# Performance work log

Hardware: AMD Instinct MI355X
Metric: run time of the kernel (lower is better)

## Reference

```python
import jax, jax.numpy as jnp
import numpy as np

N_GROUPS = 32
N_HEADS = 8
GN_EPS = 1e-5


def setup_inputs() -> dict:
    key = jax.random.key(0)
    k1, k2, k3 = jax.random.split(key, 3)
    B, C, H, W = 8, 512, 32, 32
    x = jax.random.normal(k1, (B, C, H, W), dtype=jnp.float32)
    gn_w = jnp.ones((C,), dtype=jnp.float32)
    gn_b = jnp.zeros((C,), dtype=jnp.float32)
    qkv_w = jax.random.normal(k2, (3 * C, C), dtype=jnp.float32) * 0.02
    qkv_b = jnp.zeros((3 * C,), dtype=jnp.float32)
    proj_w = jax.random.normal(k3, (C, C), dtype=jnp.float32) * 0.02
    proj_b = jnp.zeros((C,), dtype=jnp.float32)
    return {"x": x, "gn_w": gn_w, "gn_b": gn_b, "qkv_w": qkv_w,
            "qkv_b": qkv_b, "proj_w": proj_w, "proj_b": proj_b}


def reference(x, gn_w, gn_b, qkv_w, qkv_b, proj_w, proj_b):
    b, c, h, w = x.shape
    t = h * w
    xf = x.reshape(b, c, t)

    # GroupNorm(32, C) over (channel-group, spatial) dims
    xg = xf.reshape(b, N_GROUPS, (c // N_GROUPS) * t)
    mean = jnp.mean(xg, axis=-1, keepdims=True)
    var = jnp.var(xg, axis=-1, keepdims=True)
    normed = ((xg - mean) * jax.lax.rsqrt(var + GN_EPS)).reshape(b, c, t)
    normed = normed * gn_w[None, :, None] + gn_b[None, :, None]

    # 1x1 Conv1d -> matmul over channel dim
    qkv = jnp.einsum('oc,bct->bot', qkv_w, normed) + qkv_b[None, :, None]
    q, k, v = jnp.split(qkv, 3, axis=1)  # each [b, c, t]

    ch = c // N_HEADS
    scale = 1.0 / np.sqrt(np.sqrt(ch)).astype(np.float32)
    q = (q * scale).reshape(b * N_HEADS, ch, t)
    k = (k * scale).reshape(b * N_HEADS, ch, t)
    v = v.reshape(b * N_HEADS, ch, t)

    weight = jnp.einsum('bct,bcs->bts', q, k)
    weight = jax.nn.softmax(weight.astype(jnp.float32), axis=-1).astype(q.dtype)
    a = jnp.einsum('bts,bcs->bct', weight, v).reshape(b, c, t)

    # residual + 1x1 Conv2d projection
    out = jnp.einsum('oc,bct->bot', proj_w, xf + a) + proj_b[None, :, None]
    return out.reshape(b, -1, h, w)
```

## Files before the change

kernel.cpp:

```cpp
#include <hip/hip_runtime.h>

constexpr int B = 8;
constexpr int C = 512;
constexpr int T = 1024;
constexpr int CPG = 16;
constexpr int NH = 8;
constexpr int CH = 64;
constexpr float GN_EPS = 1e-5f;
constexpr float SCALE = 0.35355339059327373f;
constexpr float QSCALE = 0.18033688011112042f;

typedef __attribute__((ext_vector_type(4))) float f32x4;
typedef __attribute__((ext_vector_type(8))) short bf16x8;
typedef __attribute__((ext_vector_type(4))) short bf16x4;

__device__ inline short f2bf(float f) {
  union { float f; unsigned u; } v; v.f = f;
  unsigned r = (v.u + 0x7FFFu + ((v.u >> 16) & 1u)) >> 16;
  return (short)r;
}

__device__ inline unsigned cvt_pk_bf16(float a, float b) {
  unsigned r;
  asm("v_cvt_pk_bf16_f32 %0, %1, %2" : "=v"(r) : "v"(a), "v"(b));
  return r;
}

#define GLOAD16(gsrc, ldst) __builtin_amdgcn_global_load_lds( \
    (const __attribute__((address_space(1))) unsigned int*)(gsrc), \
    (__attribute__((address_space(3))) unsigned int*)(ldst), 16, 0, 0)

__global__ __launch_bounds__(256)
void wconv_kernel(const float* __restrict__ qw, const float* __restrict__ pw,
                  short* __restrict__ qwb, short* __restrict__ pwb) {
  const int idx = blockIdx.x * 256 + threadIdx.x;
  constexpr int QW4 = 3 * C * C / 4;
  float4 v;
  short* dst;
  if (idx < QW4) {
    v = ((const float4*)qw)[idx];
    dst = qwb + (size_t)idx * 4;
  } else {
    v = ((const float4*)pw)[idx - QW4];
    dst = pwb + (size_t)(idx - QW4) * 4;
  }
  bf16x4 o;
  o[0] = f2bf(v.x); o[1] = f2bf(v.y); o[2] = f2bf(v.z); o[3] = f2bf(v.w);
  *(bf16x4*)dst = o;
}

__global__ __launch_bounds__(256)
void gn_kernel(const float* __restrict__ x, const float* __restrict__ gw,
               const float* __restrict__ gb, short* __restrict__ out) {
  const int b = blockIdx.x >> 5;
  const int g = blockIdx.x & 31;
  const float* xp = x + (size_t)(b * C + g * CPG) * T;
  const float4* x4 = (const float4*)xp;
  float s = 0.f, ss = 0.f;
  for (int i = threadIdx.x; i < CPG * T / 4; i += 256) {
    float4 v = x4[i];
    s  += v.x + v.y + v.z + v.w;
    ss += v.x * v.x + v.y * v.y + v.z * v.z + v.w * v.w;
  }
  #pragma unroll
  for (int o = 32; o; o >>= 1) {
    s  += __shfl_down(s, o);
    ss += __shfl_down(ss, o);
  }
  __shared__ float rs[4], rss[4];
  __shared__ float sm, sr;
  const int wid = threadIdx.x >> 6;
  if ((threadIdx.x & 63) == 0) { rs[wid] = s; rss[wid] = ss; }
  __syncthreads();
  if (threadIdx.x == 0) {
    float ts  = rs[0] + rs[1] + rs[2] + rs[3];
    float tss = rss[0] + rss[1] + rss[2] + rss[3];
    constexpr float inv_n = 1.f / (CPG * T);
    float mean = ts * inv_n;
    float var = tss * inv_n - mean * mean;
    sm = mean;
    sr = rsqrtf(var + GN_EPS);
  }
  __syncthreads();
  const float mean = sm, rstd = sr;

  const int tid = threadIdx.x;
  const int cl = tid >> 4;
  const int t4 = (tid & 15) * 4;
  const float cw = gw[g * CPG + cl] * rstd;
  const float cb = gb[g * CPG + cl] - mean * cw;
  __shared__ short tile[64][20];
  const int tr = tid >> 2;
  const int cq = (tid & 3) * 4;
  for (int t0 = 0; t0 < T; t0 += 64) {
    float4 v = x4[(cl * T + t0 + t4) >> 2];
    tile[t4 + 0][cl] = f2bf(v.x * cw + cb);
    tile[t4 + 1][cl] = f2bf(v.y * cw + cb);
    tile[t4 + 2][cl] = f2bf(v.z * cw + cb);
    tile[t4 + 3][cl] = f2bf(v.w * cw + cb);
    __syncthreads();
    *(bf16x4*)&out[((size_t)(b * T + t0 + tr)) * C + g * CPG + cq] =
        *(const bf16x4*)&tile[tr][cq];
    __syncthreads();
  }
}

__global__ __launch_bounds__(256)
void qkv_gemm(const short* __restrict__ Wb, const float* __restrict__ bias,
              const short* __restrict__ Xn, short* __restrict__ qb,
              short* __restrict__ kb, short* __restrict__ vb) {
  const int b = blockIdx.z;
  const int o0 = blockIdx.y * 128;
  const int t0 = blockIdx.x * 128;
  const bool swap = (o0 >= 2 * C);
  __shared__ short Asm[128 * 64];
  __shared__ short Bsm[128 * 64];
  const int tid = threadIdx.x;
  const int wv = tid >> 6, lane = tid & 63;
  const int l15 = lane & 15, l4 = lane >> 4;
  const int wr = (wv >> 1) * 64, wc = (wv & 1) * 64;

  const short* gA[4]; const short* gB[4];
  char* lA[4]; char* lB[4];
  #pragma unroll
  for (int p = 0; p < 4; ++p) {
    const int off = p * 256 + tid;
    const int row = off >> 3;
    const int col = (off & 7) ^ (row & 7);
    gA[p] = Wb + (size_t)(o0 + row) * C + col * 8;
    gB[p] = Xn + ((size_t)b * T + t0 + row) * C + col * 8;
    lA[p] = (char*)Asm + (size_t)(p * 256 + (tid & ~63)) * 16;
    lB[p] = (char*)Bsm + (size_t)(p * 256 + (tid & ~63)) * 16;
  }

  f32x4 acc[4][4];
  #pragma unroll
  for (int i = 0; i < 4; ++i)
    #pragma unroll
    for (int j = 0; j < 4; ++j) acc[i][j] = f32x4{0.f, 0.f, 0.f, 0.f};

  for (int k0 = 0; k0 < C; k0 += 64) {
    #pragma unroll
    for (int p = 0; p < 4; ++p) {
      GLOAD16(gA[p] + k0, lA[p]);
      GLOAD16(gB[p] + k0, lB[p]);
    }
    __syncthreads();
    #pragma unroll
    for (int kk = 0; kk < 2; ++kk) {
      bf16x8 af[4], bfr[4];
      #pragma unroll
      for (int i = 0; i < 4; ++i) {
        const int sw = ((kk << 2) | l4) ^ (l15 & 7);
        af[i]  = *(const bf16x8*)&Asm[(wr + i * 16 + l15) * 64 + sw * 8];
        bfr[i] = *(const bf16x8*)&Bsm[(wc + i * 16 + l15) * 64 + sw * 8];
      }
      if (!swap) {
        #pragma unroll
        for (int fi = 0; fi < 4; ++fi)
          #pragma unroll
          for (int nj = 0; nj < 4; ++nj)
            acc[fi][nj] = __builtin_amdgcn_mfma_f32_16x16x32_bf16(
                af[fi], bfr[nj], acc[fi][nj], 0, 0, 0);
      } else {
        #pragma unroll
        for (int nj = 0; nj < 4; ++nj)
          #pragma unroll
          for (int fi = 0; fi < 4; ++fi)
            acc[nj][fi] = __builtin_amdgcn_mfma_f32_16x16x32_bf16(
                bfr[nj], af[fi], acc[nj][fi], 0, 0, 0);
      }
    }
    __syncthreads();
  }

  if (!swap) {
    short* dst = (o0 < C) ? qb : kb;
    const float sc = (o0 < C) ? QSCALE : 1.0f;
    #pragma unroll
    for (int fi = 0; fi < 4; ++fi) {
      const int ob = o0 + wr + fi * 16 + l4 * 4;
      const int bh = b * NH + ((ob >> 6) & 7);
      const int cb_ = ob & 63;
      #pragma unroll
      for (int nj = 0; nj < 4; ++nj) {
        const int tg = t0 + wc + nj * 16 + l15;
        bf16x4 pk;
        #pragma unroll
        for (int r = 0; r < 4; ++r)
          pk[r] = f2bf((acc[fi][nj][r] + bias[ob + r]) * sc);
        *(bf16x4*)&dst[((size_t)bh * T + tg) * CH + cb_] = pk;
      }
    }
  } else {
    #pragma unroll
    for (int fi = 0; fi < 4; ++fi) {
      const int ob = o0 + wr + fi * 16 + l15;
      const int bh = b * NH + ((ob >> 6) & 7);
      const int cb_ = ob & 63;
      const float bo = bias[ob];
      #pragma unroll
      for (int nj = 0; nj < 4; ++nj) {
        const int tg = t0 + wc + nj * 16 + l4 * 4;
        bf16x4 pk;
        #pragma unroll
        for (int r = 0; r < 4; ++r)
          pk[r] = f2bf(acc[nj][fi][r] + bo);
        *(bf16x4*)&vb[((size_t)bh * CH + cb_) * T + tg] = pk;
      }
    }
  }
}

__global__ __launch_bounds__(256)
void attn_kernel(const short* __restrict__ qb, const short* __restrict__ kb,
                 const short* __restrict__ vb, const float* __restrict__ x,
                 short* __restrict__ res) {
  const int linear = blockIdx.x;
  const int bh = (linear & 7) * 8 + ((linear >> 3) >> 4);
  const int tile = (linear >> 3) & 15;
  const int b = bh >> 3, h = bh & 7;
  const int t0 = tile * 64;
  const int tid = threadIdx.x;
  const int wv = tid >> 6;
  const int lane = tid & 63;
  const int l15 = lane & 15;
  const int l4 = lane >> 4;

  const short* qh = qb + (size_t)bh * T * CH;
  const short* kh = kb + (size_t)bh * T * CH;
  const short* vh = vb + (size_t)bh * CH * T;

  __shared__ short kt[2][64][64];
  __shared__ short vt[2][64][64];
  __shared__ short pl[4][16][64];
  short* plw = &pl[wv][0][0];

  const int sl_row[2] = { (0 * 256 + tid) >> 3, (1 * 256 + tid) >> 3 };
  const int sl_blk[2] = { (tid & 7) ^ (sl_row[0] & 7), (tid & 7) ^ (sl_row[1] & 7) };
  const int sl_lds[2] = { (0 * 256 + (tid & ~63)) * 8, (1 * 256 + (tid & ~63)) * 8 };

  bf16x8 qf[2];
  #pragma unroll
  for (int ks = 0; ks < 2; ++ks)
    qf[ks] = *(const bf16x8*)&qh[(size_t)(t0 + wv * 16 + l15) * CH + ks * 32 + l4 * 8];

  f32x4 acc_o[4];
  #pragma unroll
  for (int ct = 0; ct < 4; ++ct) acc_o[ct] = f32x4{0.f, 0.f, 0.f, 0.f};
  float lsum = 0.f;

  #pragma unroll
  for (int p = 0; p < 2; ++p) {
    GLOAD16(kh + (size_t)sl_row[p] * CH + sl_blk[p] * 8, &kt[0][0][0] + sl_lds[p]);
    GLOAD16(vh + (size_t)sl_row[p] * T + sl_blk[p] * 8, &vt[0][0][0] + sl_lds[p]);
  }

  for (int it = 0; it < 16; ++it) {
    const int cur = it & 1;
    __syncthreads();
    if (it < 15) {
      const int s1 = (it + 1) * 64;
      #pragma unroll
      for (int p = 0; p < 2; ++p) {
        GLOAD16(kh + (size_t)(s1 + sl_row[p]) * CH + sl_blk[p] * 8,
                &kt[cur ^ 1][0][0] + sl_lds[p]);
        GLOAD16(vh + (size_t)sl_row[p] * T + s1 + sl_blk[p] * 8,
                &vt[cur ^ 1][0][0] + sl_lds[p]);
      }
    }
    const short* ktc = &kt[cur][0][0];
    const short* vtc = &vt[cur][0][0];

    f32x4 accs[4];
    #pragma unroll
    for (int nt = 0; nt < 4; ++nt) accs[nt] = f32x4{0.f, 0.f, 0.f, 0.f};
    __builtin_amdgcn_s_setprio(1);
    #pragma unroll
    for (int ks = 0; ks < 2; ++ks) {
      #pragma unroll
      for (int nt = 0; nt < 4; ++nt) {
        bf16x8 kf = *(const bf16x8*)
            &ktc[(nt * 16 + l15) * 64 + (((ks << 2) | l4) ^ (l15 & 7)) * 8];
        accs[nt] = __builtin_amdgcn_mfma_f32_16x16x32_bf16(kf, qf[ks], accs[nt], 0, 0, 0);
      }
    }
    __builtin_amdgcn_s_setprio(0);

    f32x4 p4[4];
    #pragma unroll
    for (int nt = 0; nt < 4; ++nt)
      #pragma unroll
      for (int r = 0; r < 4; ++r)
        p4[nt][r] = __builtin_amdgcn_exp2f(accs[nt][r]);

    {
      f32x4 sv;
      #pragma unroll
      for (int r = 0; r < 4; ++r)
        sv[r] = (p4[0][r] + p4[1][r]) + (p4[2][r] + p4[3][r]);
      lsum += (sv[0] + sv[1]) + (sv[2] + sv[3]);
    }

    #pragma unroll
    for (int nt = 0; nt < 4; ++nt) {
      uint2 w;
      w.x = cvt_pk_bf16(p4[nt][0], p4[nt][1]);
      w.y = cvt_pk_bf16(p4[nt][2], p4[nt][3]);
      *(uint2*)&plw[l15 * 64 + ((nt * 2 + (l4 >> 1)) ^ (l15 & 7)) * 8 + (l4 & 1) * 4] = w;
    }

    __builtin_amdgcn_s_setprio(1);
    #pragma unroll
    for (int ks = 0; ks < 2; ++ks) {
      bf16x8 pf = *(const bf16x8*)
          &plw[l15 * 64 + (((ks << 2) | l4) ^ (l15 & 7)) * 8];
      #pragma unroll
      for (int ct = 0; ct < 4; ++ct) {
        bf16x8 vf = *(const bf16x8*)
            &vtc[(ct * 16 + l15) * 64 + (((ks << 2) | l4) ^ (l15 & 7)) * 8];
        acc_o[ct] = __builtin_amdgcn_mfma_f32_16x16x32_bf16(vf, pf, acc_o[ct], 0, 0, 0);
      }
    }
    __builtin_amdgcn_s_setprio(0);
  }

  float l = lsum;
  l += __shfl_xor(l, 16);
  l += __shfl_xor(l, 32);

  const float inv = 1.f / l;
  const int trow = t0 + wv * 16 + l15;
  #pragma unroll
  for (int ct = 0; ct < 4; ++ct) {
    const int cbase = h * CH + ct * 16 + l4 * 4;
    bf16x4 pk;
    #pragma unroll
    for (int r = 0; r < 4; ++r) {
      const float xv = x[((size_t)(b * C + cbase + r)) * T + trow];
      pk[r] = f2bf(acc_o[ct][r] * inv + xv);
    }
    *(bf16x4*)&res[((size_t)(b * T + trow)) * C + cbase] = pk;
  }
}

__global__ __launch_bounds__(256)
void proj_gemm(const short* __restrict__ Wp, const float* __restrict__ bias,
               const short* __restrict__ Rs, float* __restrict__ out) {
  const int b = blockIdx.z;
  const int o0 = blockIdx.y * 128;
  const int t0 = blockIdx.x * 128;
  __shared__ short Asm[128 * 64];
  __shared__ short Bsm[128 * 64];
  const int tid = threadIdx.x;
  const int wv = tid >> 6, lane = tid & 63;
  const int l15 = lane & 15, l4 = lane >> 4;
  const int wr = (wv >> 1) * 64, wc = (wv & 1) * 64;

  const short* gA[4]; const short* gB[4];
  char* lA[4]; char* lB[4];
  #pragma unroll
  for (int p = 0; p < 4; ++p) {
    const int off = p * 256 + tid;
    const int row = off >> 3;
    const int col = (off & 7) ^ (row & 7);
    gA[p] = Wp + (size_t)(o0 + row) * C + col * 8;
    gB[p] = Rs + ((size_t)b * T + t0 + row) * C + col * 8;
    lA[p] = (char*)Asm + (size_t)(p * 256 + (tid & ~63)) * 16;
    lB[p] = (char*)Bsm + (size_t)(p * 256 + (tid & ~63)) * 16;
  }

  f32x4 acc[4][4];
  #pragma unroll
  for (int i = 0; i < 4; ++i)
    #pragma unroll
    for (int j = 0; j < 4; ++j) acc[i][j] = f32x4{0.f, 0.f, 0.f, 0.f};

  for (int k0 = 0; k0 < C; k0 += 64) {
    #pragma unroll
    for (int p = 0; p < 4; ++p) {
      GLOAD16(gA[p] + k0, lA[p]);
      GLOAD16(gB[p] + k0, lB[p]);
    }
    __syncthreads();
    #pragma unroll
    for (int kk = 0; kk < 2; ++kk) {
      bf16x8 af[4], bfr[4];
      #pragma unroll
      for (int i = 0; i < 4; ++i) {
        const int sw = ((kk << 2) | l4) ^ (l15 & 7);
        af[i]  = *(const bf16x8*)&Asm[(wr + i * 16 + l15) * 64 + sw * 8];
        bfr[i] = *(const bf16x8*)&Bsm[(wc + i * 16 + l15) * 64 + sw * 8];
      }
      #pragma unroll
      for (int nj = 0; nj < 4; ++nj)
        #pragma unroll
        for (int fi = 0; fi < 4; ++fi)
          acc[nj][fi] = __builtin_amdgcn_mfma_f32_16x16x32_bf16(
              bfr[nj], af[fi], acc[nj][fi], 0, 0, 0);
    }
    __syncthreads();
  }

  #pragma unroll
  for (int fi = 0; fi < 4; ++fi) {
    const int o = o0 + wr + fi * 16 + l15;
    const float bo = bias[o];
    #pragma unroll
    for (int nj = 0; nj < 4; ++nj) {
      const int tg = t0 + wc + nj * 16 + l4 * 4;
      f32x4 vo;
      #pragma unroll
      for (int r = 0; r < 4; ++r) vo[r] = acc[nj][fi][r] + bo;
      *(f32x4*)&out[((size_t)(b * C + o)) * T + tg] = vo;
    }
  }
}

extern "C" void kernel_launch(void* const* d_in, const int* in_sizes, int n_in,
                              void* d_out, int out_size, void* d_ws, size_t ws_size,
                              hipStream_t stream) {
  const float* x      = (const float*)d_in[0];
  const float* gn_w   = (const float*)d_in[1];
  const float* gn_b   = (const float*)d_in[2];
  const float* qkv_w  = (const float*)d_in[3];
  const float* qkv_b  = (const float*)d_in[4];
  const float* proj_w = (const float*)d_in[5];
  const float* proj_b = (const float*)d_in[6];
  float* out = (float*)d_out;

  constexpr size_t MB = 1 << 20;
  char* w = (char*)d_ws;
  short* normed = (short*)w;
  short* qbuf   = (short*)(w + 8 * MB);
  short* kbuf   = (short*)(w + 16 * MB);
  short* vbuf   = (short*)(w + 24 * MB);
  short* resb   = (short*)(w + 32 * MB);
  short* qwb    = (short*)(w + 40 * MB);
  short* pwb    = (short*)(w + 40 * MB + (size_t)3 * C * C * 2);

  wconv_kernel<<<dim3(1024), 256, 0, stream>>>(qkv_w, proj_w, qwb, pwb);
  gn_kernel<<<dim3(B * 32), 256, 0, stream>>>(x, gn_w, gn_b, normed);
  qkv_gemm<<<dim3(T / 128, 3 * C / 128, B), 256, 0, stream>>>(qwb, qkv_b, normed,
                                                              qbuf, kbuf, vbuf);
  attn_kernel<<<dim3(B * NH * (T / 64)), 256, 0, stream>>>(qbuf, kbuf, vbuf, x, resb);
  proj_gemm<<<dim3(T / 128, C / 128, B), 256, 0, stream>>>(pwb, proj_b, resb, out);
}
```

Measured before the change: 92.56 us.

## Double-buffer GEMM LDS tiles and double query rows per attention wave

Both the QKV and projection GEMMs now double-buffer their A/B LDS tiles, prefetching the next K slice while MFMAs run on the current one, and raise wave priority around the MFMA blocks. The attention kernel now has each wave handle 32 query rows (two 16-row fragments) instead of 16. Each K/V tile loaded into LDS is therefore reused twice as much, and the grid is halved. The costs are double the LDS per GEMM block, more registers and LDS for the attention kernel, and fewer attention blocks to spread across the CUs.

```diff
diff --git a/kernel.cpp b/kernel.cpp
--- a/kernel.cpp
+++ b/kernel.cpp
@@ -7,7 +7,6 @@
 constexpr int NH = 8;
 constexpr int CH = 64;
 constexpr float GN_EPS = 1e-5f;
-constexpr float SCALE = 0.35355339059327373f;
 constexpr float QSCALE = 0.18033688011112042f;
 
 typedef __attribute__((ext_vector_type(4))) float f32x4;
@@ -113,8 +112,8 @@
   const int o0 = blockIdx.y * 128;
   const int t0 = blockIdx.x * 128;
   const bool swap = (o0 >= 2 * C);
-  __shared__ short Asm[128 * 64];
-  __shared__ short Bsm[128 * 64];
+  __shared__ short Asm[2][128 * 64];
+  __shared__ short Bsm[2][128 * 64];
   const int tid = threadIdx.x;
   const int wv = tid >> 6, lane = tid & 63;
   const int l15 = lane & 15, l4 = lane >> 4;
@@ -129,8 +128,8 @@
     const int col = (off & 7) ^ (row & 7);
     gA[p] = Wb + (size_t)(o0 + row) * C + col * 8;
     gB[p] = Xn + ((size_t)b * T + t0 + row) * C + col * 8;
-    lA[p] = (char*)Asm + (size_t)(p * 256 + (tid & ~63)) * 16;
-    lB[p] = (char*)Bsm + (size_t)(p * 256 + (tid & ~63)) * 16;
+    lA[p] = (char*)&Asm[0][0] + (size_t)(p * 256 + (tid & ~63)) * 16;
+    lB[p] = (char*)&Bsm[0][0] + (size_t)(p * 256 + (tid & ~63)) * 16;
   }
 
   f32x4 acc[4][4];
@@ -139,22 +138,35 @@
     #pragma unroll
     for (int j = 0; j < 4; ++j) acc[i][j] = f32x4{0.f, 0.f, 0.f, 0.f};
 
-  for (int k0 = 0; k0 < C; k0 += 64) {
-    #pragma unroll
-    for (int p = 0; p < 4; ++p) {
-      GLOAD16(gA[p] + k0, lA[p]);
-      GLOAD16(gB[p] + k0, lB[p]);
-    }
-    __syncthreads();
+  #pragma unroll
+  for (int p = 0; p < 4; ++p) {
+    GLOAD16(gA[p], lA[p]);
+    GLOAD16(gB[p], lB[p]);
+  }
+  __syncthreads();
+
+  int cur = 0;
+  for (int ks = 0; ks < 8; ++ks) {
+    if (ks < 7) {
+      const int k0n = (ks + 1) * 64;
+      #pragma unroll
+      for (int p = 0; p < 4; ++p) {
+        GLOAD16(gA[p] + k0n, lA[p] + (cur ^ 1) * 16384);
+        GLOAD16(gB[p] + k0n, lB[p] + (cur ^ 1) * 16384);
+      }
+    }
+    const short* As = &Asm[cur][0];
+    const short* Bs = &Bsm[cur][0];
     #pragma unroll
     for (int kk = 0; kk < 2; ++kk) {
       bf16x8 af[4], bfr[4];
       #pragma unroll
       for (int i = 0; i < 4; ++i) {
         const int sw = ((kk << 2) | l4) ^ (l15 & 7);
-        af[i]  = *(const bf16x8*)&Asm[(wr + i * 16 + l15) * 64 + sw * 8];
-        bfr[i] = *(const bf16x8*)&Bsm[(wc + i * 16 + l15) * 64 + sw * 8];
-      }
+        af[i]  = *(const bf16x8*)&As[(wr + i * 16 + l15) * 64 + sw * 8];
+        bfr[i] = *(const bf16x8*)&Bs[(wc + i * 16 + l15) * 64 + sw * 8];
+      }
+      __builtin_amdgcn_s_setprio(1);
       if (!swap) {
         #pragma unroll
         for (int fi = 0; fi < 4; ++fi)
@@ -170,8 +182,10 @@
             acc[nj][fi] = __builtin_amdgcn_mfma_f32_16x16x32_bf16(
                 bfr[nj], af[fi], acc[nj][fi], 0, 0, 0);
       }
+      __builtin_amdgcn_s_setprio(0);
     }
     __syncthreads();
+    cur ^= 1;
   }
 
   if (!swap) {
@@ -216,11 +230,10 @@
 void attn_kernel(const short* __restrict__ qb, const short* __restrict__ kb,
                  const short* __restrict__ vb, const float* __restrict__ x,
                  short* __restrict__ res) {
-  const int linear = blockIdx.x;
-  const int bh = (linear & 7) * 8 + ((linear >> 3) >> 4);
-  const int tile = (linear >> 3) & 15;
+  const int bh = blockIdx.x & 63;
+  const int tile = blockIdx.x >> 6;
   const int b = bh >> 3, h = bh & 7;
-  const int t0 = tile * 64;
+  const int t0 = tile * 128;
   const int tid = threadIdx.x;
   const int wv = tid >> 6;
   const int lane = tid & 63;
@@ -233,27 +246,32 @@
 
   __shared__ short kt[2][64][64];
   __shared__ short vt[2][64][64];
-  __shared__ short pl[4][16][64];
-  short* plw = &pl[wv][0][0];
+  __shared__ short pl[4][2][16][64];
+  short* plw = &pl[wv][0][0][0];
 
   const int sl_row[2] = { (0 * 256 + tid) >> 3, (1 * 256 + tid) >> 3 };
   const int sl_blk[2] = { (tid & 7) ^ (sl_row[0] & 7), (tid & 7) ^ (sl_row[1] & 7) };
   const int sl_lds[2] = { (0 * 256 + (tid & ~63)) * 8, (1 * 256 + (tid & ~63)) * 8 };
 
-  bf16x8 qf[2];
-  #pragma unroll
-  for (int ks = 0; ks < 2; ++ks)
-    qf[ks] = *(const bf16x8*)&qh[(size_t)(t0 + wv * 16 + l15) * CH + ks * 32 + l4 * 8];
-
-  f32x4 acc_o[4];
-  #pragma unroll
-  for (int ct = 0; ct < 4; ++ct) acc_o[ct] = f32x4{0.f, 0.f, 0.f, 0.f};
-  float lsum = 0.f;
+  bf16x8 qf[2][2];
+  #pragma unroll
+  for (int nj = 0; nj < 2; ++nj)
+    #pragma unroll
+    for (int ks = 0; ks < 2; ++ks)
+      qf[nj][ks] = *(const bf16x8*)
+          &qh[(size_t)(t0 + wv * 32 + nj * 16 + l15) * CH + ks * 32 + l4 * 8];
+
+  f32x4 acc_o[2][4];
+  #pragma unroll
+  for (int nj = 0; nj < 2; ++nj)
+    #pragma unroll
+    for (int ct = 0; ct < 4; ++ct) acc_o[nj][ct] = f32x4{0.f, 0.f, 0.f, 0.f};
+  float lsum[2] = {0.f, 0.f};
 
   #pragma unroll
   for (int p = 0; p < 2; ++p) {
-    GLOAD16(kh + (size_t)sl_row[p] * CH + sl_blk[p] * 8, &kt[0][0][0] + sl_lds[p]);
-    GLOAD16(vh + (size_t)sl_row[p] * T + sl_blk[p] * 8, &vt[0][0][0] + sl_lds[p]);
+    GLOAD16(kh + (size_t)sl_row[p] * CH + sl_blk[p] * 8, (char*)&kt[0][0][0] + sl_lds[p] * 2);
+    GLOAD16(vh + (size_t)sl_row[p] * T + sl_blk[p] * 8, (char*)&vt[0][0][0] + sl_lds[p] * 2);
   }
 
   for (int it = 0; it < 16; ++it) {
@@ -264,17 +282,19 @@
       #pragma unroll
       for (int p = 0; p < 2; ++p) {
         GLOAD16(kh + (size_t)(s1 + sl_row[p]) * CH + sl_blk[p] * 8,
-                &kt[cur ^ 1][0][0] + sl_lds[p]);
+                (char*)&kt[cur ^ 1][0][0] + sl_lds[p] * 2);
         GLOAD16(vh + (size_t)sl_row[p] * T + s1 + sl_blk[p] * 8,
-                &vt[cur ^ 1][0][0] + sl_lds[p]);
+                (char*)&vt[cur ^ 1][0][0] + sl_lds[p] * 2);
       }
     }
     const short* ktc = &kt[cur][0][0];
     const short* vtc = &vt[cur][0][0];
 
-    f32x4 accs[4];
-    #pragma unroll
-    for (int nt = 0; nt < 4; ++nt) accs[nt] = f32x4{0.f, 0.f, 0.f, 0.f};
+    f32x4 accs[2][4];
+    #pragma unroll
+    for (int nj = 0; nj < 2; ++nj)
+      #pragma unroll
+      for (int nt = 0; nt < 4; ++nt) accs[nj][nt] = f32x4{0.f, 0.f, 0.f, 0.f};
     __builtin_amdgcn_s_setprio(1);
     #pragma unroll
     for (int ks = 0; ks < 2; ++ks) {
@@ -282,65 +302,70 @@
       for (int nt = 0; nt < 4; ++nt) {
         bf16x8 kf = *(const bf16x8*)
             &ktc[(nt * 16 + l15) * 64 + (((ks << 2) | l4) ^ (l15 & 7)) * 8];
-        accs[nt] = __builtin_amdgcn_mfma_f32_16x16x32_bf16(kf, qf[ks], accs[nt], 0, 0, 0);
+        accs[0][nt] = __builtin_amdgcn_mfma_f32_16x16x32_bf16(kf, qf[0][ks], accs[0][nt], 0, 0, 0);
+        accs[1][nt] = __builtin_amdgcn_mfma_f32_16x16x32_bf16(kf, qf[1][ks], accs[1][nt], 0, 0, 0);
       }
     }
     __builtin_amdgcn_s_setprio(0);
 
-    f32x4 p4[4];
-    #pragma unroll
-    for (int nt = 0; nt < 4; ++nt)
+    f32x4 p4[2][4];
+    #pragma unroll
+    for (int nj = 0; nj < 2; ++nj) {
+      #pragma unroll
+      for (int nt = 0; nt < 4; ++nt)
+        #pragma unroll
+        for (int r = 0; r < 4; ++r)
+          p4[nj][nt][r] = __builtin_amdgcn_exp2f(accs[nj][nt][r]);
+      f32x4 sv;
       #pragma unroll
       for (int r = 0; r < 4; ++r)
-        p4[nt][r] = __builtin_amdgcn_exp2f(accs[nt][r]);
-
-    {
-      f32x4 sv;
-      #pragma unroll
-      for (int r = 0; r < 4; ++r)
-        sv[r] = (p4[0][r] + p4[1][r]) + (p4[2][r] + p4[3][r]);
-      lsum += (sv[0] + sv[1]) + (sv[2] + sv[3]);
-    }
-
-    #pragma unroll
-    for (int nt = 0; nt < 4; ++nt) {
-      uint2 w;
-      w.x = cvt_pk_bf16(p4[nt][0], p4[nt][1]);
-      w.y = cvt_pk_bf16(p4[nt][2], p4[nt][3]);
-      *(uint2*)&plw[l15 * 64 + ((nt * 2 + (l4 >> 1)) ^ (l15 & 7)) * 8 + (l4 & 1) * 4] = w;
+        sv[r] = (p4[nj][0][r] + p4[nj][1][r]) + (p4[nj][2][r] + p4[nj][3][r]);
+      lsum[nj] += (sv[0] + sv[1]) + (sv[2] + sv[3]);
+      #pragma unroll
+      for (int nt = 0; nt < 4; ++nt) {
+        uint2 w;
+        w.x = cvt_pk_bf16(p4[nj][nt][0], p4[nj][nt][1]);
+        w.y = cvt_pk_bf16(p4[nj][nt][2], p4[nj][nt][3]);
+        *(uint2*)&plw[nj * 1024 + l15 * 64 +
+                      ((nt * 2 + (l4 >> 1)) ^ (l15 & 7)) * 8 + (l4 & 1) * 4] = w;
+      }
     }
 
     __builtin_amdgcn_s_setprio(1);
     #pragma unroll
     for (int ks = 0; ks < 2; ++ks) {
-      bf16x8 pf = *(const bf16x8*)
-          &plw[l15 * 64 + (((ks << 2) | l4) ^ (l15 & 7)) * 8];
+      const int psl = (((ks << 2) | l4) ^ (l15 & 7)) * 8;
+      bf16x8 pf0 = *(const bf16x8*)&plw[l15 * 64 + psl];
+      bf16x8 pf1 = *(const bf16x8*)&plw[1024 + l15 * 64 + psl];
       #pragma unroll
       for (int ct = 0; ct < 4; ++ct) {
         bf16x8 vf = *(const bf16x8*)
             &vtc[(ct * 16 + l15) * 64 + (((ks << 2) | l4) ^ (l15 & 7)) * 8];
-        acc_o[ct] = __builtin_amdgcn_mfma_f32_16x16x32_bf16(vf, pf, acc_o[ct], 0, 0, 0);
+        acc_o[0][ct] = __builtin_amdgcn_mfma_f32_16x16x32_bf16(vf, pf0, acc_o[0][ct], 0, 0, 0);
+        acc_o[1][ct] = __builtin_amdgcn_mfma_f32_16x16x32_bf16(vf, pf1, acc_o[1][ct], 0, 0, 0);
       }
     }
     __builtin_amdgcn_s_setprio(0);
   }
 
-  float l = lsum;
-  l += __shfl_xor(l, 16);
-  l += __shfl_xor(l, 32);
-
-  const float inv = 1.f / l;
-  const int trow = t0 + wv * 16 + l15;
-  #pragma unroll
-  for (int ct = 0; ct < 4; ++ct) {
-    const int cbase = h * CH + ct * 16 + l4 * 4;
-    bf16x4 pk;
-    #pragma unroll
-    for (int r = 0; r < 4; ++r) {
-      const float xv = x[((size_t)(b * C + cbase + r)) * T + trow];
-      pk[r] = f2bf(acc_o[ct][r] * inv + xv);
-    }
-    *(bf16x4*)&res[((size_t)(b * T + trow)) * C + cbase] = pk;
+  #pragma unroll
+  for (int nj = 0; nj < 2; ++nj) {
+    float l = lsum[nj];
+    l += __shfl_xor(l, 16);
+    l += __shfl_xor(l, 32);
+    const float inv = 1.f / l;
+    const int trow = t0 + wv * 32 + nj * 16 + l15;
+    #pragma unroll
+    for (int ct = 0; ct < 4; ++ct) {
+      const int cbase = h * CH + ct * 16 + l4 * 4;
+      bf16x4 pk;
+      #pragma unroll
+      for (int r = 0; r < 4; ++r) {
+        const float xv = x[((size_t)(b * C + cbase + r)) * T + trow];
+        pk[r] = f2bf(acc_o[nj][ct][r] * inv + xv);
+      }
+      *(bf16x4*)&res[((size_t)(b * T + trow)) * C + cbase] = pk;
+    }
   }
 }
 
@@ -350,8 +375,8 @@
   const int b = blockIdx.z;
   const int o0 = blockIdx.y * 128;
   const int t0 = blockIdx.x * 128;
-  __shared__ short Asm[128 * 64];
-  __shared__ short Bsm[128 * 64];
+  __shared__ short Asm[2][128 * 64];
+  __shared__ short Bsm[2][128 * 64];
   const int tid = threadIdx.x;
   const int wv = tid >> 6, lane = tid & 63;
   const int l15 = lane & 15, l4 = lane >> 4;
@@ -366,8 +391,8 @@
     const int col = (off & 7) ^ (row & 7);
     gA[p] = Wp + (size_t)(o0 + row) * C + col * 8;
     gB[p] = Rs + ((size_t)b * T + t0 + row) * C + col * 8;
-    lA[p] = (char*)Asm + (size_t)(p * 256 + (tid & ~63)) * 16;
-    lB[p] = (char*)Bsm + (size_t)(p * 256 + (tid & ~63)) * 16;
+    lA[p] = (char*)&Asm[0][0] + (size_t)(p * 256 + (tid & ~63)) * 16;
+    lB[p] = (char*)&Bsm[0][0] + (size_t)(p * 256 + (tid & ~63)) * 16;
   }
 
   f32x4 acc[4][4];
@@ -376,30 +401,45 @@
     #pragma unroll
     for (int j = 0; j < 4; ++j) acc[i][j] = f32x4{0.f, 0.f, 0.f, 0.f};
 
-  for (int k0 = 0; k0 < C; k0 += 64) {
-    #pragma unroll
-    for (int p = 0; p < 4; ++p) {
-      GLOAD16(gA[p] + k0, lA[p]);
-      GLOAD16(gB[p] + k0, lB[p]);
-    }
-    __syncthreads();
+  #pragma unroll
+  for (int p = 0; p < 4; ++p) {
+    GLOAD16(gA[p], lA[p]);
+    GLOAD16(gB[p], lB[p]);
+  }
+  __syncthreads();
+
+  int cur = 0;
+  for (int ks = 0; ks < 8; ++ks) {
+    if (ks < 7) {
+      const int k0n = (ks + 1) * 64;
+      #pragma unroll
+      for (int p = 0; p < 4; ++p) {
+        GLOAD16(gA[p] + k0n, lA[p] + (cur ^ 1) * 16384);
+        GLOAD16(gB[p] + k0n, lB[p] + (cur ^ 1) * 16384);
+      }
+    }
+    const short* As = &Asm[cur][0];
+    const short* Bs = &Bsm[cur][0];
     #pragma unroll
     for (int kk = 0; kk < 2; ++kk) {
       bf16x8 af[4], bfr[4];
       #pragma unroll
       for (int i = 0; i < 4; ++i) {
         const int sw = ((kk << 2) | l4) ^ (l15 & 7);
-        af[i]  = *(const bf16x8*)&Asm[(wr + i * 16 + l15) * 64 + sw * 8];
-        bfr[i] = *(const bf16x8*)&Bsm[(wc + i * 16 + l15) * 64 + sw * 8];
-      }
+        af[i]  = *(const bf16x8*)&As[(wr + i * 16 + l15) * 64 + sw * 8];
+        bfr[i] = *(const bf16x8*)&Bs[(wc + i * 16 + l15) * 64 + sw * 8];
+      }
+      __builtin_amdgcn_s_setprio(1);
       #pragma unroll
       for (int nj = 0; nj < 4; ++nj)
         #pragma unroll
         for (int fi = 0; fi < 4; ++fi)
           acc[nj][fi] = __builtin_amdgcn_mfma_f32_16x16x32_bf16(
               bfr[nj], af[fi], acc[nj][fi], 0, 0, 0);
+      __builtin_amdgcn_s_setprio(0);
     }
     __syncthreads();
+    cur ^= 1;
   }
 
   #pragma unroll
@@ -443,6 +483,6 @@
   gn_kernel<<<dim3(B * 32), 256, 0, stream>>>(x, gn_w, gn_b, normed);
   qkv_gemm<<<dim3(T / 128, 3 * C / 128, B), 256, 0, stream>>>(qwb, qkv_b, normed,
                                                               qbuf, kbuf, vbuf);
-  attn_kernel<<<dim3(B * NH * (T / 64)), 256, 0, stream>>>(qbuf, kbuf, vbuf, x, resb);
+  attn_kernel<<<dim3(B * NH * (T / 128)), 256, 0, stream>>>(qbuf, kbuf, vbuf, x, resb);
   proj_gemm<<<dim3(T / 128, C / 128, B), 256, 0, stream>>>(pwb, proj_b, resb, out);
 }
```

Result: no change. 93.59 us (+1.1%).
